# Kernel optimization log

Measured on AMD Instinct MI355X. Metric: run time of the kernel, lower is better.

Reference implementation:

```python
import jax, jax.numpy as jnp
import numpy as np

B = 2097152

# battery constants (from initBatteryParams)
R_GAS = 8.3144621
F_CONST = 96487.0
ALPHA = 0.5
SN, SP = 0.000437545, 0.00030962
KN, KP = 2120.96, 248898.0
RO = 0.117215
T_DIFF = 7.0e6
T_O, T_SN, T_SP = 6.08671, 1001.38, 46.4311
U0P, U0N = 4.03, 0.01
DT = 1.0
Q_MAX = 7600.0 / 0.6
VOL = 2e-5
VOL_S = 0.1 * VOL
VOL_B = VOL - VOL_S
Q_S_MAX = Q_MAX * VOL_S / VOL
AP = (-31593.7, 0.106747, 24606.4, -78561.9, 13317.9, 307387.0, 84916.1,
      -1074690.0, 2285.04, 990894.0, 283920.0, -161513.0, -469218.0)
AN = (86.19, 0.0, 0.0, 0.0, 0.0, 0.0, 0.0, 0.0, 0.0, 0.0, 0.0, 0.0, 0.0)


def _ve_sum(x, A):
    """sum_k A[k]*((2x-1)^(k+1) - 2xk(1-x)*(2x-1)^(k-1))/F, reusing powers of m=2x-1."""
    m = 2.0 * x - 1.0
    s = A[0] * m
    pw = jnp.ones_like(m)  # m^(k-1)
    m2 = m * m
    tx = 2.0 * x * (1.0 - x)
    for k in range(1, 13):
        s = s + A[k] * pw * (m2 - tx * k)
        pw = pw * m
    return s / F_CONST


def setup_inputs() -> dict:
    key = jax.random.key(0)
    k1, k2 = jax.random.split(key)
    # nominal initial state: Tb, Vo, Vsn, Vsp, qnBMax, qnSMax, qpBMin, qpSMin
    X0 = np.array([292.1, 0.0, 0.0, 0.0,
                   Q_MAX * 0.6 * VOL_B / VOL, Q_MAX * 0.6 * VOL_S / VOL,
                   Q_MAX * 0.4 * VOL_B / VOL, Q_MAX * 0.4 * VOL_S / VOL],
                  dtype=np.float32)
    pert = 1.0 + 0.02 * (jax.random.uniform(k1, (B, 8)) - 0.5)
    states = (jnp.asarray(X0)[None, :] * pert).astype(jnp.float32)
    inputs = (1.0 + 2.0 * jax.random.uniform(k2, (B, 1))).astype(jnp.float32)
    return {"inputs": inputs, "states": states}


def reference(inputs, states):
    Tb, Vo, Vsn, Vsp = states[:, 0], states[:, 1], states[:, 2], states[:, 3]
    qnB, qnS, qpB, qpS = states[:, 4], states[:, 5], states[:, 6], states[:, 7]
    i = inputs[:, 0]

    # ---- getNextState ----
    xnS = qnS / Q_S_MAX
    xpS = qpS / Q_S_MAX
    qdDn = (qnB / VOL_B - qnS / VOL_S) / T_DIFF
    qdDp = (qpB / VOL_B - qpS / VOL_S) / T_DIFF
    Jn0 = KN * jnp.power(1.0 - xnS, ALPHA) * jnp.power(xnS, ALPHA)
    Jp0 = KP * jnp.power(1.0 - xpS, ALPHA) * jnp.power(xpS, ALPHA)
    Jn = i / SN
    Jp = i / SP
    VsnNom = R_GAS * Tb / F_CONST / ALPHA * jnp.arcsinh(Jn / (2.0 * Jn0))
    VspNom = R_GAS * Tb / F_CONST / ALPHA * jnp.arcsinh(Jp / (2.0 * Jp0))

    Tb_n = Tb  # Tbdot = 0
    Vo_n = Vo + (i * RO - Vo) / T_O * DT
    Vsn_n = Vsn + (VsnNom - Vsn) / T_SN * DT
    Vsp_n = Vsp + (VspNom - Vsp) / T_SP * DT
    qnB_n = qnB - qdDn * DT
    qnS_n = qnS + (qdDn - i) * DT
    qpB_n = qpB - qdDp * DT
    qpS_n = qpS + (i + qdDp) * DT
    X_next = jnp.stack([Tb_n, Vo_n, Vsn_n, Vsp_n, qnB_n, qnS_n, qpB_n, qpS_n], axis=1)

    # ---- getNextOutput (uses next state) ----
    xnS2 = qnS_n / Q_S_MAX
    xpS2 = qpS_n / Q_S_MAX
    Ven = U0N + R_GAS * Tb_n / F_CONST * jnp.log((1.0 - xnS2) / xnS2) + _ve_sum(xnS2, AN)
    Vep = U0P + R_GAS * Tb_n / F_CONST * jnp.log((1.0 - xpS2) / xpS2) + _ve_sum(xpS2, AP)
    V = Vep - Ven - Vo_n - Vsn_n - Vsp_n
    Z = jnp.stack([Tb_n - 273.15, V], axis=1)
    return Z, X_next
```

## Files before the change

### kernel.cpp

```cpp
#include <hip/hip_runtime.h>
#include <math.h>

#define RG_F     (8.3144621f / 96487.0f)
#define INV_F    (1.0f / 96487.0f)
#define INV_SN   (1.0f / 0.000437545f)
#define INV_SP   (1.0f / 0.00030962f)
#define KN_C     2120.96f
#define KP_C     248898.0f
#define RO_C     0.117215f
#define INV_TDIFF (1.0f / 7000000.0f)
#define INV_TO   (1.0f / 6.08671f)
#define INV_TSN  (1.0f / 1001.38f)
#define INV_TSP  (1.0f / 46.4311f)
#define U0P_C    4.03f
#define U0N_C    0.01f
#define INV_VOLB (1.0f / 1.8e-05f)
#define INV_VOLS (1.0f / 2.0e-06f)
#define INV_QSMAX (1.0f / 1266.6666666666667f)
#define LN2_F    0.6931471805599453f

__device__ __forceinline__ float hrcp(float x)  { return __builtin_amdgcn_rcpf(x); }
__device__ __forceinline__ float hlog(float x)  { return __builtin_amdgcn_logf(x) * LN2_F; }
__device__ __forceinline__ float hsqrt(float x) { return __builtin_amdgcn_sqrtf(x); }

__device__ __forceinline__ float fast_asinh(float x) {
    float ax = fabsf(x);
    float r  = hlog(ax + hsqrt(fmaf(ax, ax, 1.0f)));
    return copysignf(r, x);
}

__device__ __forceinline__ float ve_sum_p(float x) {
    const float A0  = -31593.7f;
    const float A1  = 0.106747f,   A2  = 24606.4f,   A3 = -78561.9f;
    const float A4  = 13317.9f,    A5  = 307387.0f,  A6 = 84916.1f;
    const float A7  = -1074690.0f, A8  = 2285.04f,   A9 = 990894.0f;
    const float A10 = 283920.0f,   A11 = -161513.0f, A12 = -469218.0f;

    float m  = 2.0f * x - 1.0f;
    float m2 = m * m;
    float tx = 2.0f * x * (1.0f - x);
    float s  = A0 * m;
    float pw = 1.0f;
    s = fmaf(A1  * pw, m2 - tx * 1.0f,  s); pw *= m;
    s = fmaf(A2  * pw, m2 - tx * 2.0f,  s); pw *= m;
    s = fmaf(A3  * pw, m2 - tx * 3.0f,  s); pw *= m;
    s = fmaf(A4  * pw, m2 - tx * 4.0f,  s); pw *= m;
    s = fmaf(A5  * pw, m2 - tx * 5.0f,  s); pw *= m;
    s = fmaf(A6  * pw, m2 - tx * 6.0f,  s); pw *= m;
    s = fmaf(A7  * pw, m2 - tx * 7.0f,  s); pw *= m;
    s = fmaf(A8  * pw, m2 - tx * 8.0f,  s); pw *= m;
    s = fmaf(A9  * pw, m2 - tx * 9.0f,  s); pw *= m;
    s = fmaf(A10 * pw, m2 - tx * 10.0f, s); pw *= m;
    s = fmaf(A11 * pw, m2 - tx * 11.0f, s); pw *= m;
    s = fmaf(A12 * pw, m2 - tx * 12.0f, s);
    return s * INV_F;
}

__device__ __forceinline__ void cell_step(float i, float4 s0, float4 s1,
                                          float2& z, float4& x0, float4& x1) {
    const float Tb  = s0.x, Vo  = s0.y, Vsn = s0.z, Vsp = s0.w;
    const float qnB = s1.x, qnS = s1.y, qpB = s1.z, qpS = s1.w;

    const float xnS = qnS * INV_QSMAX;
    const float xpS = qpS * INV_QSMAX;

    const float qdDn = (qnB * INV_VOLB - qnS * INV_VOLS) * INV_TDIFF;
    const float qdDp = (qpB * INV_VOLB - qpS * INV_VOLS) * INV_TDIFF;

    const float Jn0 = KN_C * hsqrt(xnS * (1.0f - xnS));
    const float Jp0 = KP_C * hsqrt(xpS * (1.0f - xpS));

    const float Jn = i * INV_SN;
    const float Jp = i * INV_SP;

    const float rtfa = 2.0f * RG_F * Tb;
    const float VsnNom = rtfa * fast_asinh(Jn * 0.5f * hrcp(Jn0));
    const float VspNom = rtfa * fast_asinh(Jp * 0.5f * hrcp(Jp0));

    const float Vo_n  = Vo  + (i * RO_C  - Vo ) * INV_TO;
    const float Vsn_n = Vsn + (VsnNom    - Vsn) * INV_TSN;
    const float Vsp_n = Vsp + (VspNom    - Vsp) * INV_TSP;
    const float qnB_n = qnB - qdDn;
    const float qnS_n = qnS + (qdDn - i);
    const float qpB_n = qpB - qdDp;
    const float qpS_n = qpS + (i + qdDp);

    const float xn2 = qnS_n * INV_QSMAX;
    const float xp2 = qpS_n * INV_QSMAX;

    const float rtf = RG_F * Tb;
    const float Ven = U0N_C + rtf * hlog((1.0f - xn2) * hrcp(xn2))
                    + 86.19f * (2.0f * xn2 - 1.0f) * INV_F;
    const float Vep = U0P_C + rtf * hlog((1.0f - xp2) * hrcp(xp2))
                    + ve_sum_p(xp2);

    const float V = Vep - Ven - Vo_n - Vsn_n - Vsp_n;

    z  = make_float2(Tb - 273.15f, V);
    x0 = make_float4(Tb, Vo_n, Vsn_n, Vsp_n);
    x1 = make_float4(qnB_n, qnS_n, qpB_n, qpS_n);
}

__global__ __launch_bounds__(256) void battery_rnn_kernel(
    const float* __restrict__ cur,
    const float* __restrict__ states,
    float* __restrict__ outZ,
    float* __restrict__ outX,
    int n)
{
    const int t   = blockIdx.x * blockDim.x + threadIdx.x;
    const int idx = t * 2;
    if (idx + 1 >= n) {
        if (idx < n) {
            float4 s0 = *reinterpret_cast<const float4*>(states + (size_t)idx * 8);
            float4 s1 = *reinterpret_cast<const float4*>(states + (size_t)idx * 8 + 4);
            float2 z; float4 x0, x1;
            cell_step(cur[idx], s0, s1, z, x0, x1);
            *reinterpret_cast<float2*>(outZ + (size_t)idx * 2) = z;
            *reinterpret_cast<float4*>(outX + (size_t)idx * 8) = x0;
            *reinterpret_cast<float4*>(outX + (size_t)idx * 8 + 4) = x1;
        }
        return;
    }

    const float2 ii = *reinterpret_cast<const float2*>(cur + idx);
    const float4 a0 = *reinterpret_cast<const float4*>(states + (size_t)idx * 8);
    const float4 a1 = *reinterpret_cast<const float4*>(states + (size_t)idx * 8 + 4);
    const float4 b0 = *reinterpret_cast<const float4*>(states + (size_t)idx * 8 + 8);
    const float4 b1 = *reinterpret_cast<const float4*>(states + (size_t)idx * 8 + 12);

    float2 za, zb; float4 xa0, xa1, xb0, xb1;
    cell_step(ii.x, a0, a1, za, xa0, xa1);
    cell_step(ii.y, b0, b1, zb, xb0, xb1);

    *reinterpret_cast<float4*>(outZ + (size_t)idx * 2) =
        make_float4(za.x, za.y, zb.x, zb.y);
    float4* xo = reinterpret_cast<float4*>(outX + (size_t)idx * 8);
    xo[0] = xa0; xo[1] = xa1; xo[2] = xb0; xo[3] = xb1;
}

extern "C" void kernel_launch(void* const* d_in, const int* in_sizes, int n_in,
                              void* d_out, int out_size, void* d_ws, size_t ws_size,
                              hipStream_t stream) {
    const float* cur    = (const float*)d_in[0];
    const float* states = (const float*)d_in[1];
    const int n = in_sizes[0];

    float* outZ = (float*)d_out;
    float* outX = (float*)d_out + 2 * (size_t)n;

    const int block = 256;
    const int nthreads = (n + 1) / 2;
    const int grid  = (nthreads + block - 1) / block;
    battery_rnn_kernel<<<grid, block, 0, stream>>>(cur, states, outZ, outX, n);
}
```

Baseline: 151.2 us.

## Stage state loads and stores through LDS for coalesced one-row-per-thread access

Each block now loads its rows' 8-float states with coalesced float4 reads into a padded LDS tile (stride 10), computes one row per thread, writes the results back into LDS, and then stores them with coalesced float4 writes. This replaces the old scheme where each thread handled two rows with strided 32-byte-per-row vector accesses. The aim is better global-memory coalescing on a bandwidth-bound kernel. In exchange it adds two block barriers and LDS traffic, and each thread now handles only one row, so the grid is twice as large.

```diff
diff --git a/kernel.cpp b/kernel.cpp
--- a/kernel.cpp
+++ b/kernel.cpp
@@ -18,6 +18,9 @@
 #define INV_VOLS (1.0f / 2.0e-06f)
 #define INV_QSMAX (1.0f / 1266.6666666666667f)
 #define LN2_F    0.6931471805599453f
+
+#define BLOCK 256
+#define LDS_STRIDE 10
 
 __device__ __forceinline__ float hrcp(float x)  { return __builtin_amdgcn_rcpf(x); }
 __device__ __forceinline__ float hlog(float x)  { return __builtin_amdgcn_logf(x) * LN2_F; }
@@ -56,51 +59,6 @@
     return s * INV_F;
 }
 
-__device__ __forceinline__ void cell_step(float i, float4 s0, float4 s1,
-                                          float2& z, float4& x0, float4& x1) {
-    const float Tb  = s0.x, Vo  = s0.y, Vsn = s0.z, Vsp = s0.w;
-    const float qnB = s1.x, qnS = s1.y, qpB = s1.z, qpS = s1.w;
-
-    const float xnS = qnS * INV_QSMAX;
-    const float xpS = qpS * INV_QSMAX;
-
-    const float qdDn = (qnB * INV_VOLB - qnS * INV_VOLS) * INV_TDIFF;
-    const float qdDp = (qpB * INV_VOLB - qpS * INV_VOLS) * INV_TDIFF;
-
-    const float Jn0 = KN_C * hsqrt(xnS * (1.0f - xnS));
-    const float Jp0 = KP_C * hsqrt(xpS * (1.0f - xpS));
-
-    const float Jn = i * INV_SN;
-    const float Jp = i * INV_SP;
-
-    const float rtfa = 2.0f * RG_F * Tb;
-    const float VsnNom = rtfa * fast_asinh(Jn * 0.5f * hrcp(Jn0));
-    const float VspNom = rtfa * fast_asinh(Jp * 0.5f * hrcp(Jp0));
-
-    const float Vo_n  = Vo  + (i * RO_C  - Vo ) * INV_TO;
-    const float Vsn_n = Vsn + (VsnNom    - Vsn) * INV_TSN;
-    const float Vsp_n = Vsp + (VspNom    - Vsp) * INV_TSP;
-    const float qnB_n = qnB - qdDn;
-    const float qnS_n = qnS + (qdDn - i);
-    const float qpB_n = qpB - qdDp;
-    const float qpS_n = qpS + (i + qdDp);
-
-    const float xn2 = qnS_n * INV_QSMAX;
-    const float xp2 = qpS_n * INV_QSMAX;
-
-    const float rtf = RG_F * Tb;
-    const float Ven = U0N_C + rtf * hlog((1.0f - xn2) * hrcp(xn2))
-                    + 86.19f * (2.0f * xn2 - 1.0f) * INV_F;
-    const float Vep = U0P_C + rtf * hlog((1.0f - xp2) * hrcp(xp2))
-                    + ve_sum_p(xp2);
-
-    const float V = Vep - Ven - Vo_n - Vsn_n - Vsp_n;
-
-    z  = make_float2(Tb - 273.15f, V);
-    x0 = make_float4(Tb, Vo_n, Vsn_n, Vsp_n);
-    x1 = make_float4(qnB_n, qnS_n, qpB_n, qpS_n);
-}
-
 __global__ __launch_bounds__(256) void battery_rnn_kernel(
     const float* __restrict__ cur,
     const float* __restrict__ states,
@@ -108,35 +66,96 @@
     float* __restrict__ outX,
     int n)
 {
-    const int t   = blockIdx.x * blockDim.x + threadIdx.x;
-    const int idx = t * 2;
-    if (idx + 1 >= n) {
-        if (idx < n) {
-            float4 s0 = *reinterpret_cast<const float4*>(states + (size_t)idx * 8);
-            float4 s1 = *reinterpret_cast<const float4*>(states + (size_t)idx * 8 + 4);
-            float2 z; float4 x0, x1;
-            cell_step(cur[idx], s0, s1, z, x0, x1);
-            *reinterpret_cast<float2*>(outZ + (size_t)idx * 2) = z;
-            *reinterpret_cast<float4*>(outX + (size_t)idx * 8) = x0;
-            *reinterpret_cast<float4*>(outX + (size_t)idx * 8 + 4) = x1;
+    __shared__ float lds[BLOCK * LDS_STRIDE];
+
+    const int tid     = threadIdx.x;
+    const int rowBase = blockIdx.x * BLOCK;
+    const int row     = rowBase + tid;
+
+    const float* gsrc = states + (size_t)rowBase * 8;
+    #pragma unroll
+    for (int k = 0; k < 2; ++k) {
+        const int c = tid + k * BLOCK;
+        const int r = c >> 1, h = c & 1;
+        if (rowBase + r < n) {
+            const float4 v = *reinterpret_cast<const float4*>(gsrc + (size_t)c * 4);
+            float* dst = &lds[r * LDS_STRIDE + h * 4];
+            reinterpret_cast<float2*>(dst)[0] = make_float2(v.x, v.y);
+            reinterpret_cast<float2*>(dst)[1] = make_float2(v.z, v.w);
         }
-        return;
     }
+    __syncthreads();
 
-    const float2 ii = *reinterpret_cast<const float2*>(cur + idx);
-    const float4 a0 = *reinterpret_cast<const float4*>(states + (size_t)idx * 8);
-    const float4 a1 = *reinterpret_cast<const float4*>(states + (size_t)idx * 8 + 4);
-    const float4 b0 = *reinterpret_cast<const float4*>(states + (size_t)idx * 8 + 8);
-    const float4 b1 = *reinterpret_cast<const float4*>(states + (size_t)idx * 8 + 12);
+    if (row < n) {
+        const float* src = &lds[tid * LDS_STRIDE];
+        const float2 p0 = reinterpret_cast<const float2*>(src)[0];
+        const float2 p1 = reinterpret_cast<const float2*>(src)[1];
+        const float2 p2 = reinterpret_cast<const float2*>(src)[2];
+        const float2 p3 = reinterpret_cast<const float2*>(src)[3];
+        const float i   = cur[row];
 
-    float2 za, zb; float4 xa0, xa1, xb0, xb1;
-    cell_step(ii.x, a0, a1, za, xa0, xa1);
-    cell_step(ii.y, b0, b1, zb, xb0, xb1);
+        const float Tb  = p0.x, Vo  = p0.y, Vsn = p1.x, Vsp = p1.y;
+        const float qnB = p2.x, qnS = p2.y, qpB = p3.x, qpS = p3.y;
 
-    *reinterpret_cast<float4*>(outZ + (size_t)idx * 2) =
-        make_float4(za.x, za.y, zb.x, zb.y);
-    float4* xo = reinterpret_cast<float4*>(outX + (size_t)idx * 8);
-    xo[0] = xa0; xo[1] = xa1; xo[2] = xb0; xo[3] = xb1;
+        const float xnS = qnS * INV_QSMAX;
+        const float xpS = qpS * INV_QSMAX;
+
+        const float qdDn = (qnB * INV_VOLB - qnS * INV_VOLS) * INV_TDIFF;
+        const float qdDp = (qpB * INV_VOLB - qpS * INV_VOLS) * INV_TDIFF;
+
+        const float Jn0 = KN_C * hsqrt(xnS * (1.0f - xnS));
+        const float Jp0 = KP_C * hsqrt(xpS * (1.0f - xpS));
+
+        const float Jn = i * INV_SN;
+        const float Jp = i * INV_SP;
+
+        const float rtfa = 2.0f * RG_F * Tb;
+        const float VsnNom = rtfa * fast_asinh(Jn * 0.5f * hrcp(Jn0));
+        const float VspNom = rtfa * fast_asinh(Jp * 0.5f * hrcp(Jp0));
+
+        const float Vo_n  = Vo  + (i * RO_C  - Vo ) * INV_TO;
+        const float Vsn_n = Vsn + (VsnNom    - Vsn) * INV_TSN;
+        const float Vsp_n = Vsp + (VspNom    - Vsp) * INV_TSP;
+        const float qnB_n = qnB - qdDn;
+        const float qnS_n = qnS + (qdDn - i);
+        const float qpB_n = qpB - qdDp;
+        const float qpS_n = qpS + (i + qdDp);
+
+        const float xn2 = qnS_n * INV_QSMAX;
+        const float xp2 = qpS_n * INV_QSMAX;
+
+        const float rtf = RG_F * Tb;
+        const float Ven = U0N_C + rtf * hlog((1.0f - xn2) * hrcp(xn2))
+                        + 86.19f * (2.0f * xn2 - 1.0f) * INV_F;
+        const float Vep = U0P_C + rtf * hlog((1.0f - xp2) * hrcp(xp2))
+                        + ve_sum_p(xp2);
+
+        const float V = Vep - Ven - Vo_n - Vsn_n - Vsp_n;
+
+        *reinterpret_cast<float2*>(outZ + (size_t)row * 2) =
+            make_float2(Tb - 273.15f, V);
+
+        float* dst = &lds[tid * LDS_STRIDE];
+        reinterpret_cast<float2*>(dst)[0] = make_float2(Tb,    Vo_n);
+        reinterpret_cast<float2*>(dst)[1] = make_float2(Vsn_n, Vsp_n);
+        reinterpret_cast<float2*>(dst)[2] = make_float2(qnB_n, qnS_n);
+        reinterpret_cast<float2*>(dst)[3] = make_float2(qpB_n, qpS_n);
+    }
+    __syncthreads();
+
+    float* gdst = outX + (size_t)rowBase * 8;
+    #pragma unroll
+    for (int k = 0; k < 2; ++k) {
+        const int c = tid + k * BLOCK;
+        const int r = c >> 1, h = c & 1;
+        if (rowBase + r < n) {
+            const float* src = &lds[r * LDS_STRIDE + h * 4];
+            const float2 a = reinterpret_cast<const float2*>(src)[0];
+            const float2 b = reinterpret_cast<const float2*>(src)[1];
+            *reinterpret_cast<float4*>(gdst + (size_t)c * 4) =
+                make_float4(a.x, a.y, b.x, b.y);
+        }
+    }
 }
 
 extern "C" void kernel_launch(void* const* d_in, const int* in_sizes, int n_in,
@@ -149,8 +168,6 @@
     float* outZ = (float*)d_out;
     float* outX = (float*)d_out + 2 * (size_t)n;
 
-    const int block = 256;
-    const int nthreads = (n + 1) / 2;
-    const int grid  = (nthreads + block - 1) / block;
-    battery_rnn_kernel<<<grid, block, 0, stream>>>(cur, states, outZ, outX, n);
+    const int grid = (n + BLOCK - 1) / BLOCK;
+    battery_rnn_kernel<<<grid, BLOCK, 0, stream>>>(cur, states, outZ, outX, n);
 }
```

Result: faster. 141.9 us (-6.2%).

## Use persistent grid-stride loop with register prefetch and nontemporal stores

Applied to the files above, without the earlier changes.

Replaces the two-rows-per-thread launch with a capped grid of 2048 blocks. Each thread walks rows in a grid-stride loop and prefetches the next row's state and current into registers while the current row is computed. Outputs are written with nontemporal stores to avoid polluting cache. The aim is to overlap memory latency with compute and cut launch and tail overhead. In exchange, per-thread loads are no longer paired, so each row is stored with separate, less wide writes.

```diff
diff --git a/kernel.cpp b/kernel.cpp
--- a/kernel.cpp
+++ b/kernel.cpp
@@ -18,6 +18,12 @@
 #define INV_VOLS (1.0f / 2.0e-06f)
 #define INV_QSMAX (1.0f / 1266.6666666666667f)
 #define LN2_F    0.6931471805599453f
+
+#define BLOCK 256
+#define NBLOCKS 2048
+
+typedef float f32x4 __attribute__((ext_vector_type(4)));
+typedef float f32x2 __attribute__((ext_vector_type(2)));
 
 __device__ __forceinline__ float hrcp(float x)  { return __builtin_amdgcn_rcpf(x); }
 __device__ __forceinline__ float hlog(float x)  { return __builtin_amdgcn_logf(x) * LN2_F; }
@@ -56,8 +62,9 @@
     return s * INV_F;
 }
 
-__device__ __forceinline__ void cell_step(float i, float4 s0, float4 s1,
-                                          float2& z, float4& x0, float4& x1) {
+__device__ __forceinline__ void cell_step_store(int row, float i, float4 s0, float4 s1,
+                                                float* __restrict__ outZ,
+                                                float* __restrict__ outX) {
     const float Tb  = s0.x, Vo  = s0.y, Vsn = s0.z, Vsp = s0.w;
     const float qnB = s1.x, qnS = s1.y, qpB = s1.z, qpS = s1.w;
 
@@ -96,9 +103,14 @@
 
     const float V = Vep - Ven - Vo_n - Vsn_n - Vsp_n;
 
-    z  = make_float2(Tb - 273.15f, V);
-    x0 = make_float4(Tb, Vo_n, Vsn_n, Vsp_n);
-    x1 = make_float4(qnB_n, qnS_n, qpB_n, qpS_n);
+    f32x2 z; z[0] = Tb - 273.15f; z[1] = V;
+    __builtin_nontemporal_store(z, reinterpret_cast<f32x2*>(outZ + (size_t)row * 2));
+
+    f32x4 x0; x0[0] = Tb;    x0[1] = Vo_n;  x0[2] = Vsn_n; x0[3] = Vsp_n;
+    f32x4 x1; x1[0] = qnB_n; x1[1] = qnS_n; x1[2] = qpB_n; x1[3] = qpS_n;
+    float* xr = outX + (size_t)row * 8;
+    __builtin_nontemporal_store(x0, reinterpret_cast<f32x4*>(xr));
+    __builtin_nontemporal_store(x1, reinterpret_cast<f32x4*>(xr + 4));
 }
 
 __global__ __launch_bounds__(256) void battery_rnn_kernel(
@@ -108,35 +120,33 @@
     float* __restrict__ outX,
     int n)
 {
-    const int t   = blockIdx.x * blockDim.x + threadIdx.x;
-    const int idx = t * 2;
-    if (idx + 1 >= n) {
-        if (idx < n) {
-            float4 s0 = *reinterpret_cast<const float4*>(states + (size_t)idx * 8);
-            float4 s1 = *reinterpret_cast<const float4*>(states + (size_t)idx * 8 + 4);
-            float2 z; float4 x0, x1;
-            cell_step(cur[idx], s0, s1, z, x0, x1);
-            *reinterpret_cast<float2*>(outZ + (size_t)idx * 2) = z;
-            *reinterpret_cast<float4*>(outX + (size_t)idx * 8) = x0;
-            *reinterpret_cast<float4*>(outX + (size_t)idx * 8 + 4) = x1;
-        }
-        return;
+    const int stride = gridDim.x * blockDim.x;
+    int i = blockIdx.x * blockDim.x + threadIdx.x;
+
+    bool v = i < n;
+    float4 a0, a1; float c;
+    if (v) {
+        const float* p = states + (size_t)i * 8;
+        a0 = *reinterpret_cast<const float4*>(p);
+        a1 = *reinterpret_cast<const float4*>(p + 4);
+        c  = cur[i];
     }
 
-    const float2 ii = *reinterpret_cast<const float2*>(cur + idx);
-    const float4 a0 = *reinterpret_cast<const float4*>(states + (size_t)idx * 8);
-    const float4 a1 = *reinterpret_cast<const float4*>(states + (size_t)idx * 8 + 4);
-    const float4 b0 = *reinterpret_cast<const float4*>(states + (size_t)idx * 8 + 8);
-    const float4 b1 = *reinterpret_cast<const float4*>(states + (size_t)idx * 8 + 12);
+    while (v) {
+        const int j = i + stride;
+        const bool vn = j < n;
+        float4 b0, b1; float cn;
+        if (vn) {
+            const float* p = states + (size_t)j * 8;
+            b0 = *reinterpret_cast<const float4*>(p);
+            b1 = *reinterpret_cast<const float4*>(p + 4);
+            cn = cur[j];
+        }
 
-    float2 za, zb; float4 xa0, xa1, xb0, xb1;
-    cell_step(ii.x, a0, a1, za, xa0, xa1);
-    cell_step(ii.y, b0, b1, zb, xb0, xb1);
+        cell_step_store(i, c, a0, a1, outZ, outX);
 
-    *reinterpret_cast<float4*>(outZ + (size_t)idx * 2) =
-        make_float4(za.x, za.y, zb.x, zb.y);
-    float4* xo = reinterpret_cast<float4*>(outX + (size_t)idx * 8);
-    xo[0] = xa0; xo[1] = xa1; xo[2] = xb0; xo[3] = xb1;
+        i = j; v = vn; a0 = b0; a1 = b1; c = cn;
+    }
 }
 
 extern "C" void kernel_launch(void* const* d_in, const int* in_sizes, int n_in,
@@ -149,8 +159,7 @@
     float* outZ = (float*)d_out;
     float* outX = (float*)d_out + 2 * (size_t)n;
 
-    const int block = 256;
-    const int nthreads = (n + 1) / 2;
-    const int grid  = (nthreads + block - 1) / block;
-    battery_rnn_kernel<<<grid, block, 0, stream>>>(cur, states, outZ, outX, n);
+    int grid = (n + BLOCK - 1) / BLOCK;
+    if (grid > NBLOCKS) grid = NBLOCKS;
+    battery_rnn_kernel<<<grid, BLOCK, 0, stream>>>(cur, states, outZ, outX, n);
 }
```

After: 147.9 us. 2.2% less time.
